# Performance work log

Measured on AMD Instinct MI355X. Metric: run time of the kernel, lower is better.

Reference implementation:

```python
import jax, jax.numpy as jnp
import numpy as np

NX = 1024
N_HEAD = 16
HEAD_DIM = NX // N_HEAD
RPE_MAX = 20
LN_EPS = 1e-5


def _layernorm(h, g, b, eps=LN_EPS):
    mu = jnp.mean(h, axis=-1, keepdims=True)
    var = jnp.var(h, axis=-1, keepdims=True)
    return (h - mu) * jax.lax.rsqrt(var + eps) * g + b


def setup_inputs() -> dict:
    key = jax.random.key(0)
    ks = jax.random.split(key, 12)
    B, S = 2, 1024
    x = jax.random.normal(ks[0], (B, S, NX), dtype=jnp.float32)
    local_info = jax.random.normal(ks[1], (B, S, NX), dtype=jnp.float32)
    attention_mask = jnp.zeros((B, 1, 1, S), dtype=jnp.float32)
    pairwise_dist = jax.random.randint(ks[2], (B, S, S), -RPE_MAX, RPE_MAX + 1, dtype=jnp.int32)
    s = 0.02
    Wqkv = jax.random.normal(ks[3], (NX, 3 * NX), dtype=jnp.float32) * s
    bqkv = jnp.zeros((3 * NX,), dtype=jnp.float32)
    Wproj = jax.random.normal(ks[4], (NX, NX), dtype=jnp.float32) * s
    bproj = jnp.zeros((NX,), dtype=jnp.float32)
    rpek = jax.random.normal(ks[5], (2 * RPE_MAX + 1, HEAD_DIM), dtype=jnp.float32) * s
    ln1_g = jnp.ones((NX,), dtype=jnp.float32)
    ln1_b = jnp.zeros((NX,), dtype=jnp.float32)
    gate_W = jax.random.normal(ks[6], (2 * NX, NX), dtype=jnp.float32) * s
    return {"x": x, "local_info": local_info, "attention_mask": attention_mask,
            "pairwise_dist": pairwise_dist, "Wqkv": Wqkv, "bqkv": bqkv,
            "Wproj": Wproj, "bproj": bproj, "rpek": rpek,
            "ln1_g": ln1_g, "ln1_b": ln1_b, "gate_W": gate_W}


def reference(x, local_info, attention_mask, pairwise_dist, Wqkv, bqkv, Wproj, bproj, rpek, ln1_g, ln1_b, gate_W):
    B, S, _ = x.shape
    qkv = x @ Wqkv + bqkv                      # [B,S,3*NX]
    q, k, v = jnp.split(qkv, 3, axis=-1)
    q = q.reshape(B, S, N_HEAD, HEAD_DIM)
    k = k.reshape(B, S, N_HEAD, HEAD_DIM)
    v = v.reshape(B, S, N_HEAD, HEAD_DIM)
    # content scores [B,H,Q,K]
    w = jnp.einsum('bqhd,bkhd->bhqk', q, k)
    # relative-position bias: embedding lookup + per-query matmul
    k_rpe = rpek[pairwise_dist + RPE_MAX]      # [B,Q,K,D]
    w_rpe = jnp.einsum('bqhd,bqkd->bhqk', q, k_rpe)
    w = (w + w_rpe) / jnp.float32(HEAD_DIM) ** 0.5
    w = w + attention_mask
    p = jax.nn.softmax(w, axis=-1)
    a = jnp.einsum('bhqk,bkhd->bqhd', p, v).reshape(B, S, NX)
    a = a @ Wproj + bproj
    # residual + LN1
    h = _layernorm(x + a, ln1_g, ln1_b)
    # gated fusion of local and global info
    z = jax.nn.sigmoid(jnp.concatenate([local_info, h], axis=-1) @ gate_W)
    out = (1.0 - z) * h + z * local_info
    return out
```

## Files before the change

### kernel.cpp

```cpp
#include <hip/hip_runtime.h>
#include <hip/hip_bf16.h>

#define SEQ 1024
#define NH 16
#define HD 64
#define NXD 1024

typedef unsigned short u16;
typedef unsigned char u8;
typedef __attribute__((ext_vector_type(8))) short short8;
typedef __attribute__((ext_vector_type(4))) float f32x4;

__device__ __forceinline__ u16 f2bf(float f) {
    __hip_bfloat16 h = __float2bfloat16(f);
    u16 u; __builtin_memcpy(&u, &h, 2); return u;
}
__device__ __forceinline__ float bf2f(u16 u) {
    __hip_bfloat16 h; __builtin_memcpy(&h, &u, 2); return __bfloat162float(h);
}

__device__ __forceinline__ void gld16(const void* g, void* l) {
    __builtin_amdgcn_global_load_lds(
        (const __attribute__((address_space(1))) void*)g,
        (__attribute__((address_space(3))) void*)l, 16, 0, 0);
}

template<int N> __device__ __forceinline__ void waitcnt_vm() {
    asm volatile("s_waitcnt vmcnt(%0)" :: "n"(N) : "memory");
}
__device__ __forceinline__ void raw_barrier() {
    asm volatile("s_barrier" ::: "memory");
}

__device__ __forceinline__ void transpose_tile(const float* __restrict__ src,
        u16* __restrict__ dst, int R, int C, int bx, int by) {
    __shared__ float tile[32][33];
    int r0 = by * 32, c0 = bx * 32;
    int tr = threadIdx.x >> 3, tc = (threadIdx.x & 7) * 4;
    float4 v = *(const float4*)(src + (size_t)(r0 + tr) * C + c0 + tc);
    tile[tr][tc+0] = v.x; tile[tr][tc+1] = v.y; tile[tr][tc+2] = v.z; tile[tr][tc+3] = v.w;
    __syncthreads();
    u16* d = dst + (size_t)(c0 + tr) * R + r0 + tc;
    #pragma unroll
    for (int j = 0; j < 4; j++) d[j] = f2bf(tile[tc+j][tr]);
}

__global__ __launch_bounds__(256) void prep_all(const float* __restrict__ x,
        const float* __restrict__ local, const int* __restrict__ pd,
        const float* __restrict__ Wqkv, const float* __restrict__ Wproj,
        const float* __restrict__ gateW,
        u16* __restrict__ xb, u16* __restrict__ gateA, u8* __restrict__ pdu8,
        u16* __restrict__ WqkvT, u16* __restrict__ WprojT, u16* __restrict__ gateWT) {
    int bid = blockIdx.x;
    if (bid < 2048) {
        int i = (bid * 256 + threadIdx.x) * 4;
        float4 v = *(const float4*)(x + i);
        xb[i+0] = f2bf(v.x); xb[i+1] = f2bf(v.y); xb[i+2] = f2bf(v.z); xb[i+3] = f2bf(v.w);
    } else if (bid < 4096) {
        int i = ((bid - 2048) * 256 + threadIdx.x) * 4;
        int row = i >> 10, c = i & 1023;
        float4 v = *(const float4*)(local + i);
        u16* d = gateA + (size_t)row * 2048 + c;
        d[0] = f2bf(v.x); d[1] = f2bf(v.y); d[2] = f2bf(v.z); d[3] = f2bf(v.w);
    } else if (bid < 6144) {
        int i = ((bid - 4096) * 256 + threadIdx.x) * 4;
        int4 v = *(const int4*)(pd + i);
        uchar4 o;
        o.x = (u8)(v.x + 20); o.y = (u8)(v.y + 20);
        o.z = (u8)(v.z + 20); o.w = (u8)(v.w + 20);
        *(uchar4*)(pdu8 + i) = o;
    } else if (bid < 9216) {
        int k = bid - 6144;  transpose_tile(Wqkv,  WqkvT,  1024, 3072, k % 96, k / 96);
    } else if (bid < 10240) {
        int k = bid - 9216;  transpose_tile(Wproj, WprojT, 1024, 1024, k % 32, k / 32);
    } else {
        int k = bid - 10240; transpose_tile(gateW, gateWT, 2048, 1024, k % 32, k / 32);
    }
}

__global__ __launch_bounds__(256) void trq_kernel(const u16* __restrict__ vb,
        u16* __restrict__ vTb, const u16* __restrict__ qb,
        const float* __restrict__ rpek, u16* __restrict__ qrpe16) {
    int bid = blockIdx.x;
    if (bid < 2048) {
        __shared__ u16 tile[32][33];
        int bh = bid >> 6, d0 = ((bid >> 5) & 1) * 32, s0 = (bid & 31) * 32;
        int tr = threadIdx.x >> 3, tc = (threadIdx.x & 7) * 4;
        const u16* s = vb + ((size_t)bh * SEQ + s0 + tr) * HD + d0 + tc;
        #pragma unroll
        for (int j = 0; j < 4; j++) tile[tr][tc+j] = s[j];
        __syncthreads();
        u16* d = vTb + ((size_t)bh * HD + d0 + tr) * SEQ + s0 + tc;
        #pragma unroll
        for (int j = 0; j < 4; j++) d[j] = tile[tc+j][tr];
    } else {
        int t = threadIdx.x, lane = t & 63, wid = t >> 6;
        int quad = lane >> 4, l16 = lane & 15;
        int r0 = ((bid - 2048) * 4 + wid) * 16;
        short8 af[2];
        #pragma unroll
        for (int s = 0; s < 2; s++)
            af[s] = *(const short8*)(qb + (size_t)(r0 + l16) * HD + s * 32 + quad * 8);
        #pragma unroll
        for (int nt = 0; nt < 3; nt++) {
            int n = nt * 16 + l16;
            const float* rp = rpek + (size_t)(n < 41 ? n : 40) * HD;
            f32x4 acc = {0.f, 0.f, 0.f, 0.f};
            #pragma unroll
            for (int s = 0; s < 2; s++) {
                float4 f0 = *(const float4*)(rp + s * 32 + quad * 8);
                float4 f1 = *(const float4*)(rp + s * 32 + quad * 8 + 4);
                short8 bf;
                bf[0] = (short)f2bf(f0.x); bf[1] = (short)f2bf(f0.y);
                bf[2] = (short)f2bf(f0.z); bf[3] = (short)f2bf(f0.w);
                bf[4] = (short)f2bf(f1.x); bf[5] = (short)f2bf(f1.y);
                bf[6] = (short)f2bf(f1.z); bf[7] = (short)f2bf(f1.w);
                acc = __builtin_amdgcn_mfma_f32_16x16x32_bf16(af[s], bf, acc, 0, 0, 0);
            }
            if (n < 41) {
                #pragma unroll
                for (int r = 0; r < 4; r++)
                    qrpe16[(size_t)(r0 + quad * 4 + r) * 48 + n] = f2bf(acc[r]);
            }
        }
    }
}

template<int BM, int BN, int EPI>
__global__ __launch_bounds__(256) void gemm_bt(
        const u16* __restrict__ A, int lda, const u16* __restrict__ BT, int K,
        const float* __restrict__ bias, float* __restrict__ out_f,
        u16* __restrict__ oq, u16* __restrict__ ok, u16* __restrict__ ov,
        const u16* __restrict__ h16, const float* __restrict__ loc32,
        float* __restrict__ outg) {
    const int LOGBM = (BM == 128) ? 7 : 6;
    const int LOGBN = (BN == 128) ? 7 : 6;
    const int MT = BM / 32, NT = BN / 32;
    const int LPT = BM / 32 + BN / 32;
    __shared__ u16 Al[2][8 * BM * 8];
    __shared__ u16 Bl[2][8 * BN * 8];
    int t = threadIdx.x, lane = t & 63, wid = t >> 6;
    int quad = lane >> 4, l16 = lane & 15;
    int m0 = blockIdx.y * BM, n0 = blockIdx.x * BN;
    int waveM = wid >> 1, waveN = wid & 1;
    f32x4 acc[MT][NT] = {};

    auto stage = [&](int buf, int k0) {
        #pragma unroll
        for (int i = 0; i < BM / 32; i++) {
            int c = t + i * 256, c0 = c & ~63;
            int m = c & (BM - 1), kb = c >> LOGBM;
            gld16(A + (size_t)(m0 + m) * lda + k0 + kb * 8,
                  &Al[buf][((c0 >> LOGBM) * BM + (c0 & (BM - 1))) * 8]);
        }
        #pragma unroll
        for (int i = 0; i < BN / 32; i++) {
            int c = t + i * 256, c0 = c & ~63;
            int n = c & (BN - 1), kb = c >> LOGBN;
            gld16(BT + (size_t)(n0 + n) * K + k0 + kb * 8,
                  &Bl[buf][((c0 >> LOGBN) * BN + (c0 & (BN - 1))) * 8]);
        }
    };

    const int NTILES = K >> 6;
    stage(0, 0);
    for (int tt = 0; tt < NTILES; tt++) {
        int cur = tt & 1;
        raw_barrier();
        if (tt + 1 < NTILES) {
            stage(cur ^ 1, (tt + 1) << 6);
            waitcnt_vm<LPT>();
        } else {
            waitcnt_vm<0>();
        }
        raw_barrier();
        const u16* Ac = Al[cur];
        const u16* Bc = Bl[cur];
        short8 af[MT][2], bfr[NT][2];
        #pragma unroll
        for (int s = 0; s < 2; s++) {
            #pragma unroll
            for (int mt = 0; mt < MT; mt++)
                af[mt][s] = *(const short8*)&Ac[((s * 4 + quad) * BM + waveM * (BM / 2) + mt * 16 + l16) * 8];
            #pragma unroll
            for (int nt = 0; nt < NT; nt++)
                bfr[nt][s] = *(const short8*)&Bc[((s * 4 + quad) * BN + waveN * (BN / 2) + nt * 16 + l16) * 8];
        }
        #pragma unroll
        for (int mt = 0; mt < MT; mt++)
            #pragma unroll
            for (int nt = 0; nt < NT; nt++) {
                acc[mt][nt] = __builtin_amdgcn_mfma_f32_16x16x32_bf16(af[mt][0], bfr[nt][0], acc[mt][nt], 0, 0, 0);
                acc[mt][nt] = __builtin_amdgcn_mfma_f32_16x16x32_bf16(af[mt][1], bfr[nt][1], acc[mt][nt], 0, 0, 0);
            }
    }
    #pragma unroll
    for (int mt = 0; mt < MT; mt++)
        #pragma unroll
        for (int nt = 0; nt < NT; nt++)
            #pragma unroll
            for (int r = 0; r < 4; r++) {
                int row = m0 + waveM * (BM / 2) + mt * 16 + quad * 4 + r;
                int col = n0 + waveN * (BN / 2) + nt * 16 + l16;
                float val = acc[mt][nt][r];
                if (EPI == 0) {
                    val += bias[col];
                    int b = row >> 10, s = row & 1023;
                    int sec = col >> 10, cc = col & 1023;
                    int h = cc >> 6, d = cc & 63;
                    u16 bv = f2bf(val);
                    size_t qidx = (((size_t)(b * NH + h)) * SEQ + s) * HD + d;
                    if (sec == 0)      oq[qidx] = bv;
                    else if (sec == 1) ok[qidx] = bv;
                    else               ov[qidx] = bv;
                } else if (EPI == 1) {
                    out_f[(size_t)row * 1024 + col] = val + bias[col];
                } else {
                    float z = 1.f / (1.f + __expf(-val));
                    size_t idx = (size_t)row * 1024 + col;
                    float hv = bf2f(h16[(size_t)row * 2048 + 1024 + col]);
                    outg[idx] = (1.f - z) * hv + z * loc32[idx];
                }
            }
}

__global__ __launch_bounds__(256) void attn_kernel(
        const u16* __restrict__ qb, const u16* __restrict__ kmat,
        const u16* __restrict__ vTb, const u16* __restrict__ qrpe16,
        const u8* __restrict__ pdu8, const float* __restrict__ mask,
        u16* __restrict__ po0, u16* __restrict__ po1, float* __restrict__ pl) {
    __shared__ u16 Kl[8 * 64 * 8];
    __shared__ u16 Vl[8 * 64 * 8];
    __shared__ u16 Pl[4][8 * 16 * 8];
    __shared__ u16 qr_lds[64 * 48];
    __shared__ u8 pdl[64 * 80];
    int t = threadIdx.x, lane = t & 63, wid = t >> 6;
    int quad = lane >> 4, l16 = lane & 15;

    int id = blockIdx.x;
    int xcd = id & 7, j = id >> 3;
    int b = xcd >> 2;
    int head = ((xcd & 3) << 2) | (j >> 5);
    int qblk = ((j >> 1) & 15) << 6;
    int sp = j & 1;
    int bh = (b << 4) | head;
    int q0 = qblk + wid * 16;

    {
        const u16* src = qrpe16 + ((size_t)bh * SEQ + qblk) * 48;
        { int c = t, c0 = c & ~63; gld16(src + (size_t)c * 8, &qr_lds[c0 * 8]); }
        if (wid < 2) { int c = 256 + t, c0 = c & ~63; gld16(src + (size_t)c * 8, &qr_lds[c0 * 8]); }
    }

    short8 aq[2];
    #pragma unroll
    for (int s = 0; s < 2; s++)
        aq[s] = *(const short8*)(qb + ((size_t)bh * SEQ + q0 + l16) * HD + s * 32 + quad * 8);
    f32x4 o[4] = {};
    float lrow[4] = {0.f, 0.f, 0.f, 0.f};
    u16* Pw = Pl[wid];
    const u8* pdbase = pdu8 + ((size_t)b * SEQ + qblk) * SEQ;
    for (int kt = 0; kt < 8; kt++) {
        int k0 = sp * 512 + kt * 64;
        __syncthreads();
        #pragma unroll
        for (int i = 0; i < 2; i++) {
            int c = t + i * 256, c0 = c & ~63;
            int s = c & 63, g = c >> 6, g0 = c0 >> 6;
            gld16(kmat + ((size_t)bh * SEQ + k0 + s) * HD + g * 8, &Kl[(g0 * 64) * 8]);
            gld16(vTb + ((size_t)bh * HD + s) * SEQ + k0 + g * 8, &Vl[(g0 * 64) * 8]);
        }
        {
            int qrow = t >> 2, kj = (t & 3) * 16;
            uint4 pv = *(const uint4*)(pdbase + (size_t)qrow * SEQ + k0 + kj);
            *(uint4*)&pdl[qrow * 80 + kj] = pv;
        }
        __syncthreads();
        #pragma unroll
        for (int ks = 0; ks < 4; ks++) {
            f32x4 a = {0.f, 0.f, 0.f, 0.f};
            #pragma unroll
            for (int dh = 0; dh < 2; dh++) {
                short8 bk = *(short8*)&Kl[((dh * 4 + quad) * 64 + ks * 16 + l16) * 8];
                a = __builtin_amdgcn_mfma_f32_16x16x32_bf16(aq[dh], bk, a, 0, 0, 0);
            }
            int kcol = k0 + ks * 16 + l16;
            float mk = mask[b * SEQ + kcol];
            int kcl = ks * 16 + l16;
            #pragma unroll
            for (int r = 0; r < 4; r++) {
                int ql = wid * 16 + quad * 4 + r;
                int pdv = pdl[ql * 80 + kcl];
                float rpe = bf2f(qr_lds[ql * 48 + pdv]);
                float sc = (a[r] + rpe) * 0.125f + mk;
                float p = __expf(fminf(sc, 30.f));
                lrow[r] += p;
                Pw[((kcl >> 3) * 16 + quad * 4 + r) * 8 + (kcl & 7)] = f2bf(p);
            }
        }
        asm volatile("s_waitcnt lgkmcnt(0)" ::: "memory");
        #pragma unroll
        for (int ks2 = 0; ks2 < 2; ks2++) {
            short8 pa = *(short8*)&Pw[((ks2 * 4 + quad) * 16 + l16) * 8];
            #pragma unroll
            for (int dt = 0; dt < 4; dt++) {
                short8 vv = *(short8*)&Vl[((ks2 * 4 + quad) * 64 + dt * 16 + l16) * 8];
                o[dt] = __builtin_amdgcn_mfma_f32_16x16x32_bf16(pa, vv, o[dt], 0, 0, 0);
            }
        }
    }
    #pragma unroll
    for (int r = 0; r < 4; r++) {
        #pragma unroll
        for (int off = 1; off < 16; off <<= 1)
            lrow[r] += __shfl_xor(lrow[r], off, 16);
    }
    u16* po = sp ? po1 : po0;
    #pragma unroll
    for (int r = 0; r < 4; r++) {
        int row = bh * SEQ + q0 + quad * 4 + r;
        #pragma unroll
        for (int dt = 0; dt < 4; dt++)
            po[(size_t)row * 64 + dt * 16 + l16] = f2bf(o[dt][r]);
        if (l16 == 0)
            pl[sp * 32768 + row] = lrow[r];
    }
}

__global__ __launch_bounds__(256) void attn_combine(const u16* __restrict__ po0,
        const u16* __restrict__ po1, const float* __restrict__ pl,
        u16* __restrict__ aoutb) {
    int idx = blockIdx.x * 256 + threadIdx.x;
    int row = idx >> 6, d = idx & 63;
    float l0 = pl[row], l1 = pl[32768 + row];
    float inv = 1.f / (l0 + l1);
    float o0 = bf2f(po0[(size_t)row * 64 + d]);
    float o1 = bf2f(po1[(size_t)row * 64 + d]);
    float val = (o0 + o1) * inv;
    int bh = row >> 10, qrow = row & 1023;
    int b = bh >> 4, h = bh & 15;
    aoutb[((size_t)(b * SEQ + qrow)) * NXD + h * HD + d] = f2bf(val);
}

__device__ __forceinline__ float block_sum(float v, float* sred) {
    #pragma unroll
    for (int o = 32; o > 0; o >>= 1) v += __shfl_down(v, o, 64);
    int lane = threadIdx.x & 63, wid = threadIdx.x >> 6;
    __syncthreads();
    if (lane == 0) sred[wid] = v;
    __syncthreads();
    return sred[0] + sred[1] + sred[2] + sred[3];
}

__global__ __launch_bounds__(256) void ln_kernel(const float* __restrict__ x,
        const float* __restrict__ a, const float* __restrict__ g,
        const float* __restrict__ bln, u16* __restrict__ gateA) {
    int row = blockIdx.x;
    __shared__ float sred[4];
    float vals[4];
    float s = 0.f;
    #pragma unroll
    for (int i = 0; i < 4; i++) {
        int c = threadIdx.x + i * 256;
        vals[i] = x[(size_t)row * NXD + c] + a[(size_t)row * NXD + c];
        s += vals[i];
    }
    s = block_sum(s, sred);
    float mu = s * (1.f / NXD);
    float vs = 0.f;
    #pragma unroll
    for (int i = 0; i < 4; i++) { float d = vals[i] - mu; vs += d * d; }
    vs = block_sum(vs, sred);
    float rstd = rsqrtf(vs * (1.f / NXD) + 1e-5f);
    #pragma unroll
    for (int i = 0; i < 4; i++) {
        int c = threadIdx.x + i * 256;
        float hv = (vals[i] - mu) * rstd * g[c] + bln[c];
        gateA[(size_t)row * 2048 + 1024 + c] = f2bf(hv);
    }
}

extern "C" void kernel_launch(void* const* d_in, const int* in_sizes, int n_in,
                              void* d_out, int out_size, void* d_ws, size_t ws_size,
                              hipStream_t stream) {
    const float* x     = (const float*)d_in[0];
    const float* local = (const float*)d_in[1];
    const float* mask  = (const float*)d_in[2];
    const int*   pd    = (const int*)d_in[3];
    const float* Wqkv  = (const float*)d_in[4];
    const float* bqkv  = (const float*)d_in[5];
    const float* Wproj = (const float*)d_in[6];
    const float* bproj = (const float*)d_in[7];
    const float* rpek  = (const float*)d_in[8];
    const float* ln_g  = (const float*)d_in[9];
    const float* ln_b  = (const float*)d_in[10];
    const float* gateW = (const float*)d_in[11];
    float* out = (float*)d_out;

    char* ws = (char*)d_ws;
    const size_t MB = 1u << 20;
    u16*   xb    = (u16*)(ws + 0);
    u16*   WqkvT = (u16*)(ws + 4 * MB);
    u16*   po0   = (u16*)(ws + 4 * MB);
    float* pl    = (float*)(ws + 8 * MB);
    u16*   WprojT= (u16*)(ws + 10 * MB);
    u16*   qb    = (u16*)(ws + 12 * MB);
    u16*   kb    = (u16*)(ws + 16 * MB);
    u16*   vb    = (u16*)(ws + 20 * MB);
    u16*   po1   = (u16*)(ws + 20 * MB);
    float* pout  = (float*)(ws + 16 * MB);
    u16*   vTb   = (u16*)(ws + 24 * MB);
    u16*   qrpe16= (u16*)(ws + 28 * MB);
    u16*   gateA = (u16*)(ws + 34 * MB);
    u8*    pdu8  = (u8*)(ws + 42 * MB);
    u16*   gateWT= (u16*)(ws + 44 * MB);
    u16*   aoutb = xb;

    prep_all<<<12288, 256, 0, stream>>>(x, local, pd, Wqkv, Wproj, gateW,
            xb, gateA, pdu8, WqkvT, WprojT, gateWT);
    gemm_bt<128, 64, 0><<<dim3(48, 16), 256, 0, stream>>>(xb, 1024, WqkvT, 1024, bqkv,
            nullptr, qb, kb, vb, nullptr, nullptr, nullptr);
    trq_kernel<<<2560, 256, 0, stream>>>(vb, vTb, qb, rpek, qrpe16);
    attn_kernel<<<1024, 256, 0, stream>>>(qb, kb, vTb, qrpe16, pdu8, mask,
            po0, po1, pl);
    attn_combine<<<8192, 256, 0, stream>>>(po0, po1, pl, aoutb);
    gemm_bt<64, 64, 1><<<dim3(16, 32), 256, 0, stream>>>(aoutb, 1024, WprojT, 1024, bproj,
            pout, nullptr, nullptr, nullptr, nullptr, nullptr, nullptr);
    ln_kernel<<<2048, 256, 0, stream>>>(x, pout, ln_g, ln_b, gateA);
    gemm_bt<64, 64, 2><<<dim3(16, 32), 256, 0, stream>>>(gateA, 2048, gateWT, 2048, nullptr,
            nullptr, nullptr, nullptr, nullptr, gateA, local, out);
}
```

Before: 258.6 us.

## Pre-swizzle GEMM operands in global memory and remap blocks to XCD-local tiles

Every producer of a GEMM operand (prep casts, weight transposes, attention combine, layernorm) now writes its bf16 rows with an XOR swizzle of the 8-element k-chunks by row. The GEMM can then load 64 contiguous k-elements per row straight into LDS and still read conflict-free via the same XOR. Block ids are also remapped so blocks landing on the same XCD cover a contiguous rectangle of output tiles, which should improve L2 reuse. The cost is a coupled layout convention across several kernels, where any mismatch silently corrupts results.

After: 226.1 us. -12.6%, faster.

```diff
diff --git a/kernel.cpp b/kernel.cpp
--- a/kernel.cpp
+++ b/kernel.cpp
@@ -31,6 +31,8 @@
 __device__ __forceinline__ void raw_barrier() {
     asm volatile("s_barrier" ::: "memory");
 }
+
+__device__ __forceinline__ int swz(int row, int k) { return k ^ ((row & 7) << 3); }
 
 __device__ __forceinline__ void transpose_tile(const float* __restrict__ src,
         u16* __restrict__ dst, int R, int C, int bx, int by) {
@@ -40,7 +42,9 @@
     float4 v = *(const float4*)(src + (size_t)(r0 + tr) * C + c0 + tc);
     tile[tr][tc+0] = v.x; tile[tr][tc+1] = v.y; tile[tr][tc+2] = v.z; tile[tr][tc+3] = v.w;
     __syncthreads();
-    u16* d = dst + (size_t)(c0 + tr) * R + r0 + tc;
+    int row = c0 + tr;
+    int kk  = r0 + tc;
+    u16* d = dst + (size_t)row * R + swz(row, kk);
     #pragma unroll
     for (int j = 0; j < 4; j++) d[j] = f2bf(tile[tc+j][tr]);
 }
@@ -54,13 +58,15 @@
     int bid = blockIdx.x;
     if (bid < 2048) {
         int i = (bid * 256 + threadIdx.x) * 4;
+        int row = i >> 10, c = i & 1023;
         float4 v = *(const float4*)(x + i);
-        xb[i+0] = f2bf(v.x); xb[i+1] = f2bf(v.y); xb[i+2] = f2bf(v.z); xb[i+3] = f2bf(v.w);
+        u16* d = xb + (size_t)row * 1024 + swz(row, c);
+        d[0] = f2bf(v.x); d[1] = f2bf(v.y); d[2] = f2bf(v.z); d[3] = f2bf(v.w);
     } else if (bid < 4096) {
         int i = ((bid - 2048) * 256 + threadIdx.x) * 4;
         int row = i >> 10, c = i & 1023;
         float4 v = *(const float4*)(local + i);
-        u16* d = gateA + (size_t)row * 2048 + c;
+        u16* d = gateA + (size_t)row * 2048 + swz(row, c);
         d[0] = f2bf(v.x); d[1] = f2bf(v.y); d[2] = f2bf(v.z); d[3] = f2bf(v.w);
     } else if (bid < 6144) {
         int i = ((bid - 4096) * 256 + threadIdx.x) * 4;
@@ -126,39 +132,39 @@
     }
 }
 
-template<int BM, int BN, int EPI>
+template<int BM, int BN, int EPI, int CHX, int CHY>
 __global__ __launch_bounds__(256) void gemm_bt(
         const u16* __restrict__ A, int lda, const u16* __restrict__ BT, int K,
         const float* __restrict__ bias, float* __restrict__ out_f,
         u16* __restrict__ oq, u16* __restrict__ ok, u16* __restrict__ ov,
         const u16* __restrict__ h16, const float* __restrict__ loc32,
         float* __restrict__ outg) {
-    const int LOGBM = (BM == 128) ? 7 : 6;
-    const int LOGBN = (BN == 128) ? 7 : 6;
     const int MT = BM / 32, NT = BN / 32;
     const int LPT = BM / 32 + BN / 32;
-    __shared__ u16 Al[2][8 * BM * 8];
-    __shared__ u16 Bl[2][8 * BN * 8];
+    __shared__ u16 Al[2][BM * 64];
+    __shared__ u16 Bl[2][BN * 64];
     int t = threadIdx.x, lane = t & 63, wid = t >> 6;
     int quad = lane >> 4, l16 = lane & 15;
-    int m0 = blockIdx.y * BM, n0 = blockIdx.x * BN;
+    int id = blockIdx.x + (CHX * 4) * blockIdx.y;
+    int xcd = id & 7, li = id >> 3;
+    int bxs = (xcd & 3) * CHX + li % CHX;
+    int bys = (xcd >> 2) * CHY + li / CHX;
+    int m0 = bys * BM, n0 = bxs * BN;
     int waveM = wid >> 1, waveN = wid & 1;
     f32x4 acc[MT][NT] = {};
 
     auto stage = [&](int buf, int k0) {
         #pragma unroll
         for (int i = 0; i < BM / 32; i++) {
-            int c = t + i * 256, c0 = c & ~63;
-            int m = c & (BM - 1), kb = c >> LOGBM;
-            gld16(A + (size_t)(m0 + m) * lda + k0 + kb * 8,
-                  &Al[buf][((c0 >> LOGBM) * BM + (c0 & (BM - 1))) * 8]);
+            int c = t + i * 256;
+            gld16(A + (size_t)(m0 + (c >> 3)) * lda + k0 + (c & 7) * 8,
+                  &Al[buf][(c & ~63) * 8]);
         }
         #pragma unroll
         for (int i = 0; i < BN / 32; i++) {
-            int c = t + i * 256, c0 = c & ~63;
-            int n = c & (BN - 1), kb = c >> LOGBN;
-            gld16(BT + (size_t)(n0 + n) * K + k0 + kb * 8,
-                  &Bl[buf][((c0 >> LOGBN) * BN + (c0 & (BN - 1))) * 8]);
+            int c = t + i * 256;
+            gld16(BT + (size_t)(n0 + (c >> 3)) * K + k0 + (c & 7) * 8,
+                  &Bl[buf][(c & ~63) * 8]);
         }
     };
 
@@ -179,12 +185,13 @@
         short8 af[MT][2], bfr[NT][2];
         #pragma unroll
         for (int s = 0; s < 2; s++) {
+            int xk = (s * 4 + quad) ^ (l16 & 7);
             #pragma unroll
             for (int mt = 0; mt < MT; mt++)
-                af[mt][s] = *(const short8*)&Ac[((s * 4 + quad) * BM + waveM * (BM / 2) + mt * 16 + l16) * 8];
+                af[mt][s] = *(const short8*)&Ac[((waveM * (BM / 2) + mt * 16 + l16) * 8 + xk) * 8];
             #pragma unroll
             for (int nt = 0; nt < NT; nt++)
-                bfr[nt][s] = *(const short8*)&Bc[((s * 4 + quad) * BN + waveN * (BN / 2) + nt * 16 + l16) * 8];
+                bfr[nt][s] = *(const short8*)&Bc[((waveN * (BN / 2) + nt * 16 + l16) * 8 + xk) * 8];
         }
         #pragma unroll
         for (int mt = 0; mt < MT; mt++)
@@ -218,7 +225,7 @@
                 } else {
                     float z = 1.f / (1.f + __expf(-val));
                     size_t idx = (size_t)row * 1024 + col;
-                    float hv = bf2f(h16[(size_t)row * 2048 + 1024 + col]);
+                    float hv = bf2f(h16[(size_t)row * 2048 + 1024 + swz(row, col)]);
                     outg[idx] = (1.f - z) * hv + z * loc32[idx];
                 }
             }
@@ -339,7 +346,8 @@
     float val = (o0 + o1) * inv;
     int bh = row >> 10, qrow = row & 1023;
     int b = bh >> 4, h = bh & 15;
-    aoutb[((size_t)(b * SEQ + qrow)) * NXD + h * HD + d] = f2bf(val);
+    int arow = b * SEQ + qrow;
+    aoutb[(size_t)arow * NXD + swz(arow, h * HD + d)] = f2bf(val);
 }
 
 __device__ __forceinline__ float block_sum(float v, float* sred) {
@@ -376,7 +384,7 @@
     for (int i = 0; i < 4; i++) {
         int c = threadIdx.x + i * 256;
         float hv = (vals[i] - mu) * rstd * g[c] + bln[c];
-        gateA[(size_t)row * 2048 + 1024 + c] = f2bf(hv);
+        gateA[(size_t)row * 2048 + 1024 + swz(row, c)] = f2bf(hv);
     }
 }
 
@@ -418,15 +426,15 @@
 
     prep_all<<<12288, 256, 0, stream>>>(x, local, pd, Wqkv, Wproj, gateW,
             xb, gateA, pdu8, WqkvT, WprojT, gateWT);
-    gemm_bt<128, 64, 0><<<dim3(48, 16), 256, 0, stream>>>(xb, 1024, WqkvT, 1024, bqkv,
+    gemm_bt<128, 64, 0, 12, 8><<<dim3(48, 16), 256, 0, stream>>>(xb, 1024, WqkvT, 1024, bqkv,
             nullptr, qb, kb, vb, nullptr, nullptr, nullptr);
     trq_kernel<<<2560, 256, 0, stream>>>(vb, vTb, qb, rpek, qrpe16);
     attn_kernel<<<1024, 256, 0, stream>>>(qb, kb, vTb, qrpe16, pdu8, mask,
             po0, po1, pl);
     attn_combine<<<8192, 256, 0, stream>>>(po0, po1, pl, aoutb);
-    gemm_bt<64, 64, 1><<<dim3(16, 32), 256, 0, stream>>>(aoutb, 1024, WprojT, 1024, bproj,
+    gemm_bt<64, 64, 1, 4, 16><<<dim3(16, 32), 256, 0, stream>>>(aoutb, 1024, WprojT, 1024, bproj,
             pout, nullptr, nullptr, nullptr, nullptr, nullptr, nullptr);
     ln_kernel<<<2048, 256, 0, stream>>>(x, pout, ln_g, ln_b, gateA);
-    gemm_bt<64, 64, 2><<<dim3(16, 32), 256, 0, stream>>>(gateA, 2048, gateWT, 2048, nullptr,
+    gemm_bt<64, 64, 2, 4, 16><<<dim3(16, 32), 256, 0, stream>>>(gateA, 2048, gateWT, 2048, nullptr,
             nullptr, nullptr, nullptr, nullptr, gateA, local, out);
 }
```
